# Optimization experiments

Measured on AMD Instinct MI355X. Metric: run time of the kernel, lower is better.

Reference implementation:

```python
import jax, jax.numpy as jnp
import numpy as np

U, I, D, E = 100000, 50000, 64, 1250000

def setup_inputs() -> dict:
    key = jax.random.key(0)
    k1, k2, k3, k4, k5 = jax.random.split(key, 5)
    return {
        "embed_user": jax.random.normal(k1, (U, D), dtype=jnp.float32),
        "embed_item": jax.random.normal(k2, (I, D), dtype=jnp.float32),
        "edge_vals": jax.random.uniform(k3, (E,), dtype=jnp.float32),
        "u_idx": jax.random.randint(k4, (E,), 0, U),
        "i_idx": jax.random.randint(k5, (E,), 0, I),
    }

def reference(embed_user, embed_item, edge_vals, u_idx, i_idx):
    # user_item_matrix @ X_items : out[u] += w_e * X_items[i_e]   -> [U, D]
    def spmm_ui(x_items):
        return jax.ops.segment_sum(edge_vals[:, None] * x_items[i_idx], u_idx,
                                   num_segments=U)
    # item_user_matrix @ X_users : out[i] += w_e * X_users[u_e]   -> [I, D]
    def spmm_iu(x_users):
        return jax.ops.segment_sum(edge_vals[:, None] * x_users[u_idx], i_idx,
                                   num_segments=I)

    gcn1_users = spmm_ui(embed_item)          # hop 1
    gcn1_items = spmm_iu(embed_user)
    gcn2_users = spmm_ui(gcn1_items)          # hop 2
    gcn2_items = spmm_iu(gcn1_users)
    gcn3_items = spmm_iu(gcn2_users)          # hop 3 (only items path is returned)

    # weighted residual sum: e + 1/2 g1 + 1/3 g2 + 1/4 g3
    gcn_items = embed_item + 0.5 * gcn1_items + (1.0 / 3.0) * gcn2_items + 0.25 * gcn3_items
    return gcn_items
```

## Files before the change

### kernel.cpp

```cpp
#include <hip/hip_runtime.h>

#define U_CNT 100000
#define I_CNT 50000
#define DIM   64
#define E_CNT 1250000

#define NB      256
#define SHIFT_U 9
#define SHIFT_I 8
#define T1      4096
#define EPT1    16
#define CAP_B   8192
#define WQBITS  15
#define CONVB   1024

typedef float floatx2 __attribute__((ext_vector_type(2)));

static __device__ __forceinline__ unsigned short f2bf(float f) {
  unsigned int u = __float_as_uint(f);
  u += 0x7fffu + ((u >> 16) & 1u);
  return (unsigned short)(u >> 16);
}
static __device__ __forceinline__ unsigned int pack_bf2(float x, float y) {
  return (unsigned int)f2bf(x) | ((unsigned int)f2bf(y) << 16);
}
static __device__ __forceinline__ unsigned int pack_fp8x4(float4 a) {
  unsigned int o = __builtin_amdgcn_cvt_pk_fp8_f32(a.x, a.y, 0u, false);
  o = __builtin_amdgcn_cvt_pk_fp8_f32(a.z, a.w, o, true);
  return o;
}

__global__ __launch_bounds__(256) void build_kernel(
    const int* __restrict__ u_idx, const int* __restrict__ i_idx,
    const float* __restrict__ vals,
    int* __restrict__ cursU, int* __restrict__ cursI,
    unsigned int* __restrict__ recsU, unsigned int* __restrict__ recsI,
    unsigned short* __restrict__ dlsU, unsigned short* __restrict__ dlsI,
    const float* __restrict__ embU, unsigned short* __restrict__ ebUb,
    const float* __restrict__ embI, unsigned short* __restrict__ ebIb,
    int E, int p1blocks) {
  __shared__ int histU[NB], histI[NB], lscanU[NB], lscanI[NB], lbaseU[NB], lbaseI[NB];
  __shared__ unsigned int stageU[T1], stageI[T1];
  __shared__ unsigned short dlstU[T1], dlstI[T1];
  __shared__ unsigned char bktU[T1], bktI[T1];
  int t = threadIdx.x;

  if (blockIdx.x >= p1blocks) {
    const int n4U = U_CNT * DIM / 4;
    const int nTot = n4U + I_CNT * DIM / 4;
    for (int i = (blockIdx.x - p1blocks) * 256 + t; i < nTot; i += CONVB * 256) {
      const float* in; unsigned short* outp; int j;
      if (i < n4U) { in = embU; outp = ebUb; j = i; }
      else         { in = embI; outp = ebIb; j = i - n4U; }
      float4 v = ((const float4*)in)[j];
      ushort4 o;
      o.x = f2bf(v.x); o.y = f2bf(v.y); o.z = f2bf(v.z); o.w = f2bf(v.w);
      ((ushort4*)outp)[j] = o;
    }
    return;
  }

  int tile0 = blockIdx.x * T1;
  int cnt = min(T1, E - tile0);

  for (int k = t; k < NB; k += 256) { histU[k] = 0; histI[k] = 0; }
  __syncthreads();

  int du[EPT1], di[EPT1]; unsigned int wq[EPT1];
#pragma unroll
  for (int k = 0; k < EPT1; ++k) {
    int s2 = k * 256 + t;
    if (s2 < cnt) {
      int e = tile0 + s2;
      du[k] = u_idx[e]; di[k] = i_idx[e];
      unsigned int wb = __float_as_uint(vals[e]);
      wq[k] = ((wb + 0x7fffu + ((wb >> 16) & 1u)) >> 16) & 0x7fffu;
      atomicAdd(&histU[du[k] >> SHIFT_U], 1);
      atomicAdd(&histI[di[k] >> SHIFT_I], 1);
    }
  }
  __syncthreads();

  int mU = histU[t], mI = histI[t];
  lbaseU[t] = t * CAP_B + (mU ? atomicAdd(&cursU[t], mU) : 0);
  lbaseI[t] = t * CAP_B + (mI ? atomicAdd(&cursI[t], mI) : 0);
  lscanU[t] = mU; lscanI[t] = mI;
  __syncthreads();
  for (int off = 1; off < NB; off <<= 1) {
    int xu = (t >= off) ? lscanU[t - off] : 0;
    int xi = (t >= off) ? lscanI[t - off] : 0;
    __syncthreads();
    if (t >= off) { lscanU[t] += xu; lscanI[t] += xi; }
    __syncthreads();
  }
  int iU = lscanU[t], iI = lscanI[t];
  __syncthreads();
  lscanU[t] = iU - mU; lscanI[t] = iI - mI;
  histU[t] = 0; histI[t] = 0;
  __syncthreads();

#pragma unroll
  for (int k = 0; k < EPT1; ++k) {
    int s2 = k * 256 + t;
    if (s2 < cnt) {
      int bU = du[k] >> SHIFT_U, bI = di[k] >> SHIFT_I;
      int pU = atomicAdd(&histU[bU], 1);
      int pI = atomicAdd(&histI[bI], 1);
      int sU = lscanU[bU] + pU, sI = lscanI[bI] + pI;
      stageU[sU] = ((unsigned int)di[k] << WQBITS) | wq[k];
      dlstU[sU] = (unsigned short)(du[k] - (bU << SHIFT_U));
      bktU[sU] = (unsigned char)bU;
      stageI[sI] = ((unsigned int)du[k] << WQBITS) | wq[k];
      dlstI[sI] = (unsigned short)(di[k] - (bI << SHIFT_I));
      bktI[sI] = (unsigned char)bI;
    }
  }
  __syncthreads();
  for (int s = t; s < cnt; s += 256) {
    int bU = bktU[s]; int gU = lbaseU[bU] + (s - lscanU[bU]);
    recsU[gU] = stageU[s]; dlsU[gU] = dlstU[s];
    int bI = bktI[s]; int gI = lbaseI[bI] + (s - lscanI[bI]);
    recsI[gI] = stageI[s]; dlsI[gI] = dlstI[s];
  }
}

__global__ __launch_bounds__(256) void csr_finalize_both(
    const int* __restrict__ cursU, const int* __restrict__ cursI,
    unsigned int* __restrict__ recsU, unsigned int* __restrict__ recsI,
    const unsigned short* __restrict__ dlsU, const unsigned short* __restrict__ dlsI,
    int2* __restrict__ rowseU, int2* __restrict__ rowseI, int nbU) {
  __shared__ int rhist[512];
  __shared__ int rscan[512];
  __shared__ int exsc[512];
  __shared__ unsigned int stage[CAP_B];
  int bb = blockIdx.x, t = threadIdx.x;
  const int* curs; unsigned int* recs; const unsigned short* dls; int2* rowse;
  int nrows, shift, b;
  if (bb < nbU) { b = bb; curs = cursU; recs = recsU; dls = dlsU; rowse = rowseU;
                  nrows = U_CNT; shift = SHIFT_U; }
  else          { b = bb - nbU; curs = cursI; recs = recsI; dls = dlsI; rowse = rowseI;
                  nrows = I_CNT; shift = SHIFT_I; }
  int rpb = 1 << shift;
  int start = b * CAP_B;
  int cnt = min(curs[b], CAP_B);
  int rowbase = b << shift;

  for (int k = t; k < rpb; k += 256) rhist[k] = 0;
  __syncthreads();
  for (int s = t; s < cnt; s += 256)
    atomicAdd(&rhist[dls[start + s]], 1);
  __syncthreads();

  for (int k = t; k < rpb; k += 256) rscan[k] = rhist[k];
  __syncthreads();
  for (int off = 1; off < rpb; off <<= 1) {
    int i0 = t, i1 = t + 256;
    int v0 = (i0 < rpb && i0 >= off) ? rscan[i0 - off] : 0;
    int v1 = (i1 < rpb && i1 >= off) ? rscan[i1 - off] : 0;
    __syncthreads();
    if (i0 < rpb && i0 >= off) rscan[i0] += v0;
    if (i1 < rpb && i1 >= off) rscan[i1] += v1;
    __syncthreads();
  }
  for (int k = t; k < rpb; k += 256) exsc[k] = rscan[k] - rhist[k];
  __syncthreads();

  for (int k = t; k < rpb; k += 256) {
    int r = rowbase + k;
    if (r < nrows) rowse[r] = make_int2(start + exsc[k], start + rscan[k]);
  }

  for (int k = t; k < rpb; k += 256) rhist[k] = 0;
  __syncthreads();
  for (int s = t; s < cnt; s += 256) {
    unsigned int rc = recs[start + s];
    int dl = dls[start + s];
    int pos = atomicAdd(&rhist[dl], 1);
    stage[exsc[dl] + pos] = rc;
  }
  __syncthreads();
  for (int s = t; s < cnt; s += 256) recs[start + s] = stage[s];
}


template <int CHUNK>
static __device__ __forceinline__ float4 gather_bf16(
    const unsigned short* __restrict__ sb,
    const unsigned int* __restrict__ recs,
    int start, int end, int sub, int q) {
  const uint2* s64 = (const uint2*)sb;
  constexpr int K = CHUNK / 4;
  float a0 = 0.f, a1 = 0.f, a2 = 0.f, a3 = 0.f;
  for (int p = start; p < end; p += CHUNK) {
    unsigned int r[K]; uint2 v[K];
#pragma unroll
    for (int k = 0; k < K; ++k) {
      int idx = p + 4 * k + q;
      r[k] = (idx < end) ? recs[idx] : 0u;
    }
#pragma unroll
    for (int k = 0; k < K; ++k)
      v[k] = s64[(size_t)(r[k] >> WQBITS) * 16 + sub];
#pragma unroll
    for (int k = 0; k < K; ++k) {
      float w = __uint_as_float((r[k] & 0x7fffu) << 16);
      a0 += w * __uint_as_float(v[k].x << 16);
      a1 += w * __uint_as_float(v[k].x & 0xffff0000u);
      a2 += w * __uint_as_float(v[k].y << 16);
      a3 += w * __uint_as_float(v[k].y & 0xffff0000u);
    }
  }
  a0 += __shfl_xor(a0, 16); a0 += __shfl_xor(a0, 32);
  a1 += __shfl_xor(a1, 16); a1 += __shfl_xor(a1, 32);
  a2 += __shfl_xor(a2, 16); a2 += __shfl_xor(a2, 32);
  a3 += __shfl_xor(a3, 16); a3 += __shfl_xor(a3, 32);
  return make_float4(a0, a1, a2, a3);
}

template <int CHUNK>
static __device__ __forceinline__ void gather_bf16_dual(
    const unsigned short* __restrict__ s1, const unsigned short* __restrict__ s2,
    const unsigned int* __restrict__ recs,
    int start, int end, int sub, int q, float4& o1, float4& o2) {
  const uint2* a64 = (const uint2*)s1;
  const uint2* b64 = (const uint2*)s2;
  constexpr int K = CHUNK / 4;
  float a0 = 0.f, a1 = 0.f, a2 = 0.f, a3 = 0.f;
  float b0 = 0.f, b1 = 0.f, b2 = 0.f, b3 = 0.f;
  for (int p = start; p < end; p += CHUNK) {
    unsigned int r[K]; uint2 v1[K], v2[K];
#pragma unroll
    for (int k = 0; k < K; ++k) {
      int idx = p + 4 * k + q;
      r[k] = (idx < end) ? recs[idx] : 0u;
    }
#pragma unroll
    for (int k = 0; k < K; ++k) {
      size_t ro = (size_t)(r[k] >> WQBITS) * 16 + sub;
      v1[k] = a64[ro];
      v2[k] = b64[ro];
    }
#pragma unroll
    for (int k = 0; k < K; ++k) {
      float w = __uint_as_float((r[k] & 0x7fffu) << 16);
      a0 += w * __uint_as_float(v1[k].x << 16);
      a1 += w * __uint_as_float(v1[k].x & 0xffff0000u);
      a2 += w * __uint_as_float(v1[k].y << 16);
      a3 += w * __uint_as_float(v1[k].y & 0xffff0000u);
      b0 += w * __uint_as_float(v2[k].x << 16);
      b1 += w * __uint_as_float(v2[k].x & 0xffff0000u);
      b2 += w * __uint_as_float(v2[k].y << 16);
      b3 += w * __uint_as_float(v2[k].y & 0xffff0000u);
    }
  }
  a0 += __shfl_xor(a0, 16); a0 += __shfl_xor(a0, 32);
  a1 += __shfl_xor(a1, 16); a1 += __shfl_xor(a1, 32);
  a2 += __shfl_xor(a2, 16); a2 += __shfl_xor(a2, 32);
  a3 += __shfl_xor(a3, 16); a3 += __shfl_xor(a3, 32);
  b0 += __shfl_xor(b0, 16); b0 += __shfl_xor(b0, 32);
  b1 += __shfl_xor(b1, 16); b1 += __shfl_xor(b1, 32);
  b2 += __shfl_xor(b2, 16); b2 += __shfl_xor(b2, 32);
  b3 += __shfl_xor(b3, 16); b3 += __shfl_xor(b3, 32);
  o1 = make_float4(a0, a1, a2, a3);
  o2 = make_float4(b0, b1, b2, b3);
}

template <int CHUNK>
static __device__ __forceinline__ void gather_fp8_dual2(
    const uint2* __restrict__ u12,
    const unsigned int* __restrict__ recs,
    int start, int end, int sub, int q, float4& o1, float4& o2) {
  constexpr int K = CHUNK / 4;
  float a0 = 0.f, a1 = 0.f, a2 = 0.f, a3 = 0.f;
  float b0 = 0.f, b1 = 0.f, b2 = 0.f, b3 = 0.f;
  for (int p = start; p < end; p += CHUNK) {
    unsigned int r[K]; uint2 v[K];
#pragma unroll
    for (int k = 0; k < K; ++k) {
      int idx = p + 4 * k + q;
      r[k] = (idx < end) ? recs[idx] : 0u;
    }
#pragma unroll
    for (int k = 0; k < K; ++k)
      v[k] = u12[(size_t)(r[k] >> WQBITS) * 16 + sub];
#pragma unroll
    for (int k = 0; k < K; ++k) {
      float w = __uint_as_float((r[k] & 0x7fffu) << 16);
      floatx2 lo = __builtin_amdgcn_cvt_pk_f32_fp8(v[k].x, false);
      floatx2 hi = __builtin_amdgcn_cvt_pk_f32_fp8(v[k].x, true);
      a0 += w * lo.x; a1 += w * lo.y; a2 += w * hi.x; a3 += w * hi.y;
      floatx2 lo2 = __builtin_amdgcn_cvt_pk_f32_fp8(v[k].y, false);
      floatx2 hi2 = __builtin_amdgcn_cvt_pk_f32_fp8(v[k].y, true);
      b0 += w * lo2.x; b1 += w * lo2.y; b2 += w * hi2.x; b3 += w * hi2.y;
    }
  }
  a0 += __shfl_xor(a0, 16); a0 += __shfl_xor(a0, 32);
  a1 += __shfl_xor(a1, 16); a1 += __shfl_xor(a1, 32);
  a2 += __shfl_xor(a2, 16); a2 += __shfl_xor(a2, 32);
  a3 += __shfl_xor(a3, 16); a3 += __shfl_xor(a3, 32);
  b0 += __shfl_xor(b0, 16); b0 += __shfl_xor(b0, 32);
  b1 += __shfl_xor(b1, 16); b1 += __shfl_xor(b1, 32);
  b2 += __shfl_xor(b2, 16); b2 += __shfl_xor(b2, 32);
  b3 += __shfl_xor(b3, 16); b3 += __shfl_xor(b3, 32);
  o1 = make_float4(a0, a1, a2, a3);
  o2 = make_float4(b0, b1, b2, b3);
}

__global__ __launch_bounds__(256) void hop1i_kernel(
    const unsigned short* __restrict__ ebU,
    const unsigned int* __restrict__ recsI, const int2* __restrict__ rowseI,
    uint2* __restrict__ i1) {
  int gw = (blockIdx.x * 256 + threadIdx.x) >> 6;
  int lane = threadIdx.x & 63;
  int sub = lane & 15, q = lane >> 4;
  if (gw >= I_CNT) return;
  int2 se = rowseI[gw];
  float4 a = gather_bf16<32>(ebU, recsI, se.x, se.y, sub, q);
  if (q == 0)
    i1[(size_t)gw * 16 + sub] = make_uint2(pack_bf2(a.x, a.y), pack_bf2(a.z, a.w));
}

__global__ __launch_bounds__(256) void hop1u_kernel(
    const unsigned short* __restrict__ ebI, const uint2* __restrict__ i1,
    const unsigned int* __restrict__ recsU, const int2* __restrict__ rowseU,
    uint2* __restrict__ u12) {
  int gw = (blockIdx.x * 256 + threadIdx.x) >> 6;
  int lane = threadIdx.x & 63;
  int sub = lane & 15, q = lane >> 4;
  if (gw >= U_CNT) return;
  int2 se = rowseU[gw];
  float4 a, b;
  gather_bf16_dual<16>(ebI, (const unsigned short*)i1, recsU, se.x, se.y, sub, q, a, b);
  if (q == 0)
    u12[(size_t)gw * 16 + sub] = make_uint2(pack_fp8x4(a), pack_fp8x4(b));
}

__global__ __launch_bounds__(256) void hop2b_kernel(
    const uint2* __restrict__ i1, const uint2* __restrict__ u12,
    const unsigned int* __restrict__ recsI, const int2* __restrict__ rowseI,
    const float* __restrict__ e_item, float* __restrict__ out) {
  int gw = (blockIdx.x * 256 + threadIdx.x) >> 6;
  int lane = threadIdx.x & 63;
  int sub = lane & 15, q = lane >> 4;
  if (gw >= I_CNT) return;
  int2 se = rowseI[gw];
  float4 a, b;
  gather_fp8_dual2<32>(u12, recsI, se.x, se.y, sub, q, a, b);
  if (q == 0) {
    size_t idx = (size_t)gw * 16 + sub;
    float4 e = ((const float4*)e_item)[idx];
    uint2 ip = i1[idx];
    const float c1 = 0.5f, c2 = (float)(1.0 / 3.0), c3 = 0.25f;
    float4 o;
    o.x = e.x + c1 * __uint_as_float(ip.x << 16)         + c2 * a.x + c3 * b.x;
    o.y = e.y + c1 * __uint_as_float(ip.x & 0xffff0000u) + c2 * a.y + c3 * b.y;
    o.z = e.z + c1 * __uint_as_float(ip.y << 16)         + c2 * a.z + c3 * b.z;
    o.w = e.w + c1 * __uint_as_float(ip.y & 0xffff0000u) + c2 * a.w + c3 * b.w;
    ((float4*)out)[idx] = o;
  }
}

extern "C" void kernel_launch(void* const* d_in, const int* in_sizes, int n_in,
                              void* d_out, int out_size, void* d_ws, size_t ws_size,
                              hipStream_t stream) {
  const float* embed_user = (const float*)d_in[0];
  const float* embed_item = (const float*)d_in[1];
  const float* edge_vals  = (const float*)d_in[2];
  const int*   u_idx      = (const int*)d_in[3];
  const int*   i_idx      = (const int*)d_in[4];
  float* out = (float*)d_out;

  auto align256 = [](size_t x) { return (x + 255) & ~(size_t)255; };
  char* ws = (char*)d_ws;
  size_t off = 0;
  const size_t capRecs = (size_t)NB * CAP_B;
  const size_t uHalf = (size_t)U_CNT * DIM * sizeof(unsigned short);
  const size_t iHalf = (size_t)I_CNT * DIM * sizeof(unsigned short);

  unsigned int* recsU = (unsigned int*)(ws + off); off += align256(capRecs * 4);
  unsigned int* recsI = (unsigned int*)(ws + off); off += align256(capRecs * 4);
  unsigned short* dlU = (unsigned short*)(ws + off); off += align256(capRecs * 2);
  unsigned short* dlI = (unsigned short*)(ws + off); off += align256(capRecs * 2);
  unsigned short* ebUb = (unsigned short*)(ws + off); off += align256(uHalf);
  unsigned short* ebIb = (unsigned short*)(ws + off); off += align256(iHalf);
  uint2* i1b = (uint2*)(ws + off); off += align256(iHalf);
  uint2* u12 = (uint2*)(ws + off); off += align256(uHalf);
  int2* rowseU = (int2*)(ws + off); off += align256((size_t)U_CNT * sizeof(int2));
  int2* rowseI = (int2*)(ws + off); off += align256((size_t)I_CNT * sizeof(int2));
  int* cursU   = (int*)(ws + off);  off += align256(2 * NB * sizeof(int));
  int* cursI   = cursU + NB;
  (void)ws_size;

  dim3 blk(256);

  hipMemsetAsync(cursU, 0, 2 * NB * sizeof(int), stream);
  const int p1blocks = (E_CNT + T1 - 1) / T1;
  build_kernel<<<p1blocks + CONVB, blk, 0, stream>>>(
      u_idx, i_idx, edge_vals, cursU, cursI, recsU, recsI, dlU, dlI,
      embed_user, ebUb, embed_item, ebIb, E_CNT, p1blocks);

  const int nbValidU = (U_CNT + (1 << SHIFT_U) - 1) >> SHIFT_U;
  const int nbValidI = (I_CNT + (1 << SHIFT_I) - 1) >> SHIFT_I;
  csr_finalize_both<<<nbValidU + nbValidI, blk, 0, stream>>>(
      cursU, cursI, recsU, recsI, dlU, dlI, rowseU, rowseI, nbValidU);

  hop1i_kernel<<<(I_CNT + 3) / 4, blk, 0, stream>>>(ebUb, recsI, rowseI, i1b);
  hop1u_kernel<<<(U_CNT + 3) / 4, blk, 0, stream>>>(ebIb, i1b, recsU, rowseU, u12);
  hop2b_kernel<<<(I_CNT + 3) / 4, blk, 0, stream>>>(i1b, u12, recsI, rowseI,
                                                    embed_item, out);
}
```

Measured before the change: 147.8 us.

## Interleave item bf16 embeddings with hop-1 results for single 16-byte gathers

The bf16 item embedding and the hop-1 item result are now stored interleaved in one array, so the hop1u gather reads both with one 16-byte load per neighbour instead of two 8-byte loads from separate arrays. The intent is fewer memory transactions and better cache-line use on the dominant random gather. The build kernel also reads edge indices and weights as int4/float4 vectors instead of scalars. The catch is that hop1i's output writes become strided and partial-line, and hop2b now reads 16 bytes where it used to read 8.

```diff
diff --git a/kernel.cpp b/kernel.cpp
--- a/kernel.cpp
+++ b/kernel.cpp
@@ -37,7 +37,7 @@
     unsigned int* __restrict__ recsU, unsigned int* __restrict__ recsI,
     unsigned short* __restrict__ dlsU, unsigned short* __restrict__ dlsI,
     const float* __restrict__ embU, unsigned short* __restrict__ ebUb,
-    const float* __restrict__ embI, unsigned short* __restrict__ ebIb,
+    const float* __restrict__ embI, uint2* __restrict__ ebIi1_2,
     int E, int p1blocks) {
   __shared__ int histU[NB], histI[NB], lscanU[NB], lscanI[NB], lbaseU[NB], lbaseI[NB];
   __shared__ unsigned int stageU[T1], stageI[T1];
@@ -49,13 +49,16 @@
     const int n4U = U_CNT * DIM / 4;
     const int nTot = n4U + I_CNT * DIM / 4;
     for (int i = (blockIdx.x - p1blocks) * 256 + t; i < nTot; i += CONVB * 256) {
-      const float* in; unsigned short* outp; int j;
-      if (i < n4U) { in = embU; outp = ebUb; j = i; }
-      else         { in = embI; outp = ebIb; j = i - n4U; }
-      float4 v = ((const float4*)in)[j];
-      ushort4 o;
-      o.x = f2bf(v.x); o.y = f2bf(v.y); o.z = f2bf(v.z); o.w = f2bf(v.w);
-      ((ushort4*)outp)[j] = o;
+      if (i < n4U) {
+        float4 v = ((const float4*)embU)[i];
+        ushort4 o;
+        o.x = f2bf(v.x); o.y = f2bf(v.y); o.z = f2bf(v.z); o.w = f2bf(v.w);
+        ((ushort4*)ebUb)[i] = o;
+      } else {
+        int j = i - n4U;
+        float4 v = ((const float4*)embI)[j];
+        ebIi1_2[2 * j] = make_uint2(pack_bf2(v.x, v.y), pack_bf2(v.z, v.w));
+      }
     }
     return;
   }
@@ -68,15 +71,23 @@
 
   int du[EPT1], di[EPT1]; unsigned int wq[EPT1];
 #pragma unroll
-  for (int k = 0; k < EPT1; ++k) {
-    int s2 = k * 256 + t;
-    if (s2 < cnt) {
-      int e = tile0 + s2;
-      du[k] = u_idx[e]; di[k] = i_idx[e];
-      unsigned int wb = __float_as_uint(vals[e]);
-      wq[k] = ((wb + 0x7fffu + ((wb >> 16) & 1u)) >> 16) & 0x7fffu;
-      atomicAdd(&histU[du[k] >> SHIFT_U], 1);
-      atomicAdd(&histI[di[k] >> SHIFT_I], 1);
+  for (int g = 0; g < EPT1 / 4; ++g) {
+    int s4 = g * 1024 + t * 4;
+    if (s4 < cnt) {
+      int e4 = (tile0 + s4) >> 2;
+      int4 uu = ((const int4*)u_idx)[e4];
+      int4 ii = ((const int4*)i_idx)[e4];
+      float4 vv = ((const float4*)vals)[e4];
+      du[4*g+0] = uu.x; du[4*g+1] = uu.y; du[4*g+2] = uu.z; du[4*g+3] = uu.w;
+      di[4*g+0] = ii.x; di[4*g+1] = ii.y; di[4*g+2] = ii.z; di[4*g+3] = ii.w;
+      const float* vp = (const float*)&vv;
+#pragma unroll
+      for (int j = 0; j < 4; ++j) {
+        unsigned int wb = __float_as_uint(vp[j]);
+        wq[4*g+j] = ((wb + 0x7fffu + ((wb >> 16) & 1u)) >> 16) & 0x7fffu;
+        atomicAdd(&histU[du[4*g+j] >> SHIFT_U], 1);
+        atomicAdd(&histI[di[4*g+j] >> SHIFT_I], 1);
+      }
     }
   }
   __syncthreads();
@@ -100,19 +111,23 @@
   __syncthreads();
 
 #pragma unroll
-  for (int k = 0; k < EPT1; ++k) {
-    int s2 = k * 256 + t;
-    if (s2 < cnt) {
-      int bU = du[k] >> SHIFT_U, bI = di[k] >> SHIFT_I;
-      int pU = atomicAdd(&histU[bU], 1);
-      int pI = atomicAdd(&histI[bI], 1);
-      int sU = lscanU[bU] + pU, sI = lscanI[bI] + pI;
-      stageU[sU] = ((unsigned int)di[k] << WQBITS) | wq[k];
-      dlstU[sU] = (unsigned short)(du[k] - (bU << SHIFT_U));
-      bktU[sU] = (unsigned char)bU;
-      stageI[sI] = ((unsigned int)du[k] << WQBITS) | wq[k];
-      dlstI[sI] = (unsigned short)(di[k] - (bI << SHIFT_I));
-      bktI[sI] = (unsigned char)bI;
+  for (int g = 0; g < EPT1 / 4; ++g) {
+    int s4 = g * 1024 + t * 4;
+    if (s4 < cnt) {
+#pragma unroll
+      for (int j = 0; j < 4; ++j) {
+        int k = 4 * g + j;
+        int bU = du[k] >> SHIFT_U, bI = di[k] >> SHIFT_I;
+        int pU = atomicAdd(&histU[bU], 1);
+        int pI = atomicAdd(&histI[bI], 1);
+        int sU = lscanU[bU] + pU, sI = lscanI[bI] + pI;
+        stageU[sU] = ((unsigned int)di[k] << WQBITS) | wq[k];
+        dlstU[sU] = (unsigned short)(du[k] - (bU << SHIFT_U));
+        bktU[sU] = (unsigned char)bU;
+        stageI[sI] = ((unsigned int)du[k] << WQBITS) | wq[k];
+        dlstI[sI] = (unsigned short)(di[k] - (bI << SHIFT_I));
+        bktI[sI] = (unsigned char)bI;
+      }
     }
   }
   __syncthreads();
@@ -218,39 +233,34 @@
 }
 
 template <int CHUNK>
-static __device__ __forceinline__ void gather_bf16_dual(
-    const unsigned short* __restrict__ s1, const unsigned short* __restrict__ s2,
+static __device__ __forceinline__ void gather_ebIi1_dual(
+    const uint4* __restrict__ s128,
     const unsigned int* __restrict__ recs,
     int start, int end, int sub, int q, float4& o1, float4& o2) {
-  const uint2* a64 = (const uint2*)s1;
-  const uint2* b64 = (const uint2*)s2;
   constexpr int K = CHUNK / 4;
   float a0 = 0.f, a1 = 0.f, a2 = 0.f, a3 = 0.f;
   float b0 = 0.f, b1 = 0.f, b2 = 0.f, b3 = 0.f;
   for (int p = start; p < end; p += CHUNK) {
-    unsigned int r[K]; uint2 v1[K], v2[K];
+    unsigned int r[K]; uint4 v[K];
 #pragma unroll
     for (int k = 0; k < K; ++k) {
       int idx = p + 4 * k + q;
       r[k] = (idx < end) ? recs[idx] : 0u;
     }
 #pragma unroll
-    for (int k = 0; k < K; ++k) {
-      size_t ro = (size_t)(r[k] >> WQBITS) * 16 + sub;
-      v1[k] = a64[ro];
-      v2[k] = b64[ro];
-    }
+    for (int k = 0; k < K; ++k)
+      v[k] = s128[(size_t)(r[k] >> WQBITS) * 16 + sub];
 #pragma unroll
     for (int k = 0; k < K; ++k) {
       float w = __uint_as_float((r[k] & 0x7fffu) << 16);
-      a0 += w * __uint_as_float(v1[k].x << 16);
-      a1 += w * __uint_as_float(v1[k].x & 0xffff0000u);
-      a2 += w * __uint_as_float(v1[k].y << 16);
-      a3 += w * __uint_as_float(v1[k].y & 0xffff0000u);
-      b0 += w * __uint_as_float(v2[k].x << 16);
-      b1 += w * __uint_as_float(v2[k].x & 0xffff0000u);
-      b2 += w * __uint_as_float(v2[k].y << 16);
-      b3 += w * __uint_as_float(v2[k].y & 0xffff0000u);
+      a0 += w * __uint_as_float(v[k].x << 16);
+      a1 += w * __uint_as_float(v[k].x & 0xffff0000u);
+      a2 += w * __uint_as_float(v[k].y << 16);
+      a3 += w * __uint_as_float(v[k].y & 0xffff0000u);
+      b0 += w * __uint_as_float(v[k].z << 16);
+      b1 += w * __uint_as_float(v[k].z & 0xffff0000u);
+      b2 += w * __uint_as_float(v[k].w << 16);
+      b3 += w * __uint_as_float(v[k].w & 0xffff0000u);
     }
   }
   a0 += __shfl_xor(a0, 16); a0 += __shfl_xor(a0, 32);
@@ -309,7 +319,7 @@
 __global__ __launch_bounds__(256) void hop1i_kernel(
     const unsigned short* __restrict__ ebU,
     const unsigned int* __restrict__ recsI, const int2* __restrict__ rowseI,
-    uint2* __restrict__ i1) {
+    uint2* __restrict__ ebIi1_2) {
   int gw = (blockIdx.x * 256 + threadIdx.x) >> 6;
   int lane = threadIdx.x & 63;
   int sub = lane & 15, q = lane >> 4;
@@ -317,11 +327,12 @@
   int2 se = rowseI[gw];
   float4 a = gather_bf16<32>(ebU, recsI, se.x, se.y, sub, q);
   if (q == 0)
-    i1[(size_t)gw * 16 + sub] = make_uint2(pack_bf2(a.x, a.y), pack_bf2(a.z, a.w));
+    ebIi1_2[2 * ((size_t)gw * 16 + sub) + 1] =
+        make_uint2(pack_bf2(a.x, a.y), pack_bf2(a.z, a.w));
 }
 
 __global__ __launch_bounds__(256) void hop1u_kernel(
-    const unsigned short* __restrict__ ebI, const uint2* __restrict__ i1,
+    const uint4* __restrict__ ebIi1,
     const unsigned int* __restrict__ recsU, const int2* __restrict__ rowseU,
     uint2* __restrict__ u12) {
   int gw = (blockIdx.x * 256 + threadIdx.x) >> 6;
@@ -330,13 +341,13 @@
   if (gw >= U_CNT) return;
   int2 se = rowseU[gw];
   float4 a, b;
-  gather_bf16_dual<16>(ebI, (const unsigned short*)i1, recsU, se.x, se.y, sub, q, a, b);
+  gather_ebIi1_dual<16>(ebIi1, recsU, se.x, se.y, sub, q, a, b);
   if (q == 0)
     u12[(size_t)gw * 16 + sub] = make_uint2(pack_fp8x4(a), pack_fp8x4(b));
 }
 
 __global__ __launch_bounds__(256) void hop2b_kernel(
-    const uint2* __restrict__ i1, const uint2* __restrict__ u12,
+    const uint4* __restrict__ ebIi1, const uint2* __restrict__ u12,
     const unsigned int* __restrict__ recsI, const int2* __restrict__ rowseI,
     const float* __restrict__ e_item, float* __restrict__ out) {
   int gw = (blockIdx.x * 256 + threadIdx.x) >> 6;
@@ -349,13 +360,13 @@
   if (q == 0) {
     size_t idx = (size_t)gw * 16 + sub;
     float4 e = ((const float4*)e_item)[idx];
-    uint2 ip = i1[idx];
+    uint4 t4 = ebIi1[idx];
     const float c1 = 0.5f, c2 = (float)(1.0 / 3.0), c3 = 0.25f;
     float4 o;
-    o.x = e.x + c1 * __uint_as_float(ip.x << 16)         + c2 * a.x + c3 * b.x;
-    o.y = e.y + c1 * __uint_as_float(ip.x & 0xffff0000u) + c2 * a.y + c3 * b.y;
-    o.z = e.z + c1 * __uint_as_float(ip.y << 16)         + c2 * a.z + c3 * b.z;
-    o.w = e.w + c1 * __uint_as_float(ip.y & 0xffff0000u) + c2 * a.w + c3 * b.w;
+    o.x = e.x + c1 * __uint_as_float(t4.z << 16)         + c2 * a.x + c3 * b.x;
+    o.y = e.y + c1 * __uint_as_float(t4.z & 0xffff0000u) + c2 * a.y + c3 * b.y;
+    o.z = e.z + c1 * __uint_as_float(t4.w << 16)         + c2 * a.z + c3 * b.z;
+    o.w = e.w + c1 * __uint_as_float(t4.w & 0xffff0000u) + c2 * a.w + c3 * b.w;
     ((float4*)out)[idx] = o;
   }
 }
@@ -375,16 +386,15 @@
   size_t off = 0;
   const size_t capRecs = (size_t)NB * CAP_B;
   const size_t uHalf = (size_t)U_CNT * DIM * sizeof(unsigned short);
-  const size_t iHalf = (size_t)I_CNT * DIM * sizeof(unsigned short);
+  const size_t iIntl = (size_t)I_CNT * 16 * sizeof(uint4);
 
   unsigned int* recsU = (unsigned int*)(ws + off); off += align256(capRecs * 4);
   unsigned int* recsI = (unsigned int*)(ws + off); off += align256(capRecs * 4);
   unsigned short* dlU = (unsigned short*)(ws + off); off += align256(capRecs * 2);
   unsigned short* dlI = (unsigned short*)(ws + off); off += align256(capRecs * 2);
   unsigned short* ebUb = (unsigned short*)(ws + off); off += align256(uHalf);
-  unsigned short* ebIb = (unsigned short*)(ws + off); off += align256(iHalf);
-  uint2* i1b = (uint2*)(ws + off); off += align256(iHalf);
-  uint2* u12 = (uint2*)(ws + off); off += align256(uHalf);
+  uint4* ebIi1 = (uint4*)(ws + off); off += align256(iIntl);
+  uint2* u12   = (uint2*)(ws + off); off += align256(uHalf);
   int2* rowseU = (int2*)(ws + off); off += align256((size_t)U_CNT * sizeof(int2));
   int2* rowseI = (int2*)(ws + off); off += align256((size_t)I_CNT * sizeof(int2));
   int* cursU   = (int*)(ws + off);  off += align256(2 * NB * sizeof(int));
@@ -397,15 +407,16 @@
   const int p1blocks = (E_CNT + T1 - 1) / T1;
   build_kernel<<<p1blocks + CONVB, blk, 0, stream>>>(
       u_idx, i_idx, edge_vals, cursU, cursI, recsU, recsI, dlU, dlI,
-      embed_user, ebUb, embed_item, ebIb, E_CNT, p1blocks);
+      embed_user, ebUb, embed_item, (uint2*)ebIi1, E_CNT, p1blocks);
 
   const int nbValidU = (U_CNT + (1 << SHIFT_U) - 1) >> SHIFT_U;
   const int nbValidI = (I_CNT + (1 << SHIFT_I) - 1) >> SHIFT_I;
   csr_finalize_both<<<nbValidU + nbValidI, blk, 0, stream>>>(
       cursU, cursI, recsU, recsI, dlU, dlI, rowseU, rowseI, nbValidU);
 
-  hop1i_kernel<<<(I_CNT + 3) / 4, blk, 0, stream>>>(ebUb, recsI, rowseI, i1b);
-  hop1u_kernel<<<(U_CNT + 3) / 4, blk, 0, stream>>>(ebIb, i1b, recsU, rowseU, u12);
-  hop2b_kernel<<<(I_CNT + 3) / 4, blk, 0, stream>>>(i1b, u12, recsI, rowseI,
+  hop1i_kernel<<<(I_CNT + 3) / 4, blk, 0, stream>>>(ebUb, recsI, rowseI,
+                                                    (uint2*)ebIi1);
+  hop1u_kernel<<<(U_CNT + 3) / 4, blk, 0, stream>>>(ebIi1, recsU, rowseU, u12);
+  hop2b_kernel<<<(I_CNT + 3) / 4, blk, 0, stream>>>(ebIi1, u12, recsI, rowseI,
                                                     embed_item, out);
 }
```

New measurement: 147.0 us (median of 2 runs). Within noise of the previous version (-0.6%).
